# Kernel tuning notes

Hardware: AMD Instinct MI355X
Metric: run time of the kernel (lower is better)

The kernel has to match this reference:

```python
import jax, jax.numpy as jnp
import numpy as np

K = 3  # polynomial filter order

def gfgcn_layer(X, S, W, h, b):
    # X: [N, in], W: [in, out], h: [K], b: [out]
    X = X @ W
    X_out = h[0] * X
    Sx = X
    for k in range(1, K):
        Sx = S @ Sx                 # graph shift propagation
        X_out = X_out + h[k] * Sx   # scalar-weighted accumulate
    return X_out + b[None, :]


def setup_inputs() -> dict:
    key = jax.random.key(0)
    ks = jax.random.split(key, 12)
    N, in_dim, hid_dim, out_dim = 8192, 512, 128, 64
    # scale S so repeated propagation stays numerically tame
    S = jax.random.normal(ks[0], (N, N), dtype=jnp.float32) / jnp.sqrt(jnp.float32(N))
    X = jax.random.normal(ks[1], (N, in_dim), dtype=jnp.float32)
    def kaiming(k, shape):
        bound = np.sqrt(6.0 / shape[0])
        return jax.random.uniform(k, shape, jnp.float32, -bound, bound)
    W1 = kaiming(ks[2], (in_dim, hid_dim))
    W2 = kaiming(ks[3], (hid_dim, hid_dim))
    W3 = kaiming(ks[4], (hid_dim, out_dim))
    h1 = jnp.ones((K,), jnp.float32)
    h2 = jnp.ones((K,), jnp.float32)
    h3 = jnp.ones((K,), jnp.float32)
    b1 = jnp.zeros((hid_dim,), jnp.float32)
    b2 = jnp.zeros((hid_dim,), jnp.float32)
    b3 = jnp.zeros((out_dim,), jnp.float32)
    return {"S": S, "X": X, "W1": W1, "h1": h1, "b1": b1,
            "W2": W2, "h2": h2, "b2": b2, "W3": W3, "h3": h3, "b3": b3}


def reference(S, X, W1, h1, b1, W2, h2, b2, W3, h3, b3):
    # layer 1 + ReLU (dropout p=0 -> identity, batch_norm=False)
    X = jax.nn.relu(gfgcn_layer(X, S, W1, h1, b1))
    # layer 2 + ReLU
    X = jax.nn.relu(gfgcn_layer(X, S, W2, h2, b2))
    # last layer, last_act = Identity
    return gfgcn_layer(X, S, W3, h3, b3)
```

## Files before the change

### kernel.cpp

```cpp
#include <hip/hip_runtime.h>


typedef __attribute__((ext_vector_type(4))) float  f32x4;
typedef __attribute__((ext_vector_type(8))) __bf16 bf16x8;
typedef __attribute__((ext_vector_type(4))) __bf16 bf16x4;

__device__ __forceinline__ void gload_lds16(const __bf16* g, __bf16* l) {
    __builtin_amdgcn_global_load_lds(
        (const __attribute__((address_space(1))) void*)g,
        (__attribute__((address_space(3))) void*)l, 16, 0, 0);
}

__global__ void cvt_f32_bf16(const float4* __restrict__ in,
                             bf16x4* __restrict__ out, int n4) {
    int i  = blockIdx.x * blockDim.x + threadIdx.x;
    int st = gridDim.x * blockDim.x;
    for (; i < n4; i += st) {
        float4 v = in[i];
        bf16x4 o;
        o[0] = (__bf16)v.x; o[1] = (__bf16)v.y;
        o[2] = (__bf16)v.z; o[3] = (__bf16)v.w;
        out[i] = o;
    }
}

__global__ void cvt_transpose(const float* __restrict__ W,
                              __bf16* __restrict__ Wt, int Kd, int Md) {
    int i = blockIdx.x * blockDim.x + threadIdx.x;
    if (i < Kd * Md) {
        int k = i / Md, m = i % Md;
        Wt[(size_t)m * Kd + k] = (__bf16)W[i];
    }
}

template<int MF, int NF, int OUTMODE>
__global__ __launch_bounds__(256)
void gemm_rd(const __bf16* __restrict__ A, const __bf16* __restrict__ Bt,
             void* __restrict__ out, int K, int Kchunk, int Mtot, int Ntot)
{
    const int lane = threadIdx.x & 63;
    const int w    = threadIdx.x >> 6;
    const int l15  = lane & 15;
    const int quad = lane >> 4;

    const int m_base = blockIdx.x * (64 * MF) + w * (16 * MF);
    const int n_base = blockIdx.y * (16 * NF);
    const int kstart = blockIdx.z * Kchunk;

    const __bf16* Ap[MF];
    #pragma unroll
    for (int mf = 0; mf < MF; mf++)
        Ap[mf] = A + (size_t)(m_base + mf * 16 + l15) * K + kstart + quad * 8;
    const __bf16* Bp[NF];
    #pragma unroll
    for (int nf = 0; nf < NF; nf++)
        Bp[nf] = Bt + (size_t)(n_base + nf * 16 + l15) * K + kstart + quad * 8;

    f32x4 acc[MF][NF];
    #pragma unroll
    for (int mf = 0; mf < MF; mf++)
        #pragma unroll
        for (int nf = 0; nf < NF; nf++)
            acc[mf][nf] = (f32x4){0.f, 0.f, 0.f, 0.f};

    #pragma unroll 2
    for (int ks = 0; ks < Kchunk; ks += 32) {
        bf16x8 a[MF], b[NF];
        #pragma unroll
        for (int mf = 0; mf < MF; mf++) a[mf] = *(const bf16x8*)(Ap[mf] + ks);
        #pragma unroll
        for (int nf = 0; nf < NF; nf++) b[nf] = *(const bf16x8*)(Bp[nf] + ks);
        #pragma unroll
        for (int mf = 0; mf < MF; mf++)
            #pragma unroll
            for (int nf = 0; nf < NF; nf++)
                acc[mf][nf] = __builtin_amdgcn_mfma_f32_16x16x32_bf16(
                    a[mf], b[nf], acc[mf][nf], 0, 0, 0);
    }

    if (OUTMODE == 0) {
        float* P = (float*)out + (size_t)blockIdx.z * Mtot * Ntot;
        #pragma unroll
        for (int mf = 0; mf < MF; mf++) {
            const int rowb = m_base + mf * 16 + quad * 4;
            #pragma unroll
            for (int nf = 0; nf < NF; nf++) {
                const int col = n_base + nf * 16 + l15;
                *(f32x4*)(P + (size_t)col * Mtot + rowb) = acc[mf][nf];
            }
        }
    } else {
        __bf16* O = (__bf16*)out;
        #pragma unroll
        for (int mf = 0; mf < MF; mf++) {
            const int rowb = m_base + mf * 16 + quad * 4;
            #pragma unroll
            for (int nf = 0; nf < NF; nf++) {
                const int col = n_base + nf * 16 + l15;
                #pragma unroll
                for (int r = 0; r < 4; r++)
                    O[(size_t)(rowb + r) * Ntot + col] = (__bf16)acc[mf][nf][r];
            }
        }
    }
}

template<int NF>
__global__ __launch_bounds__(256)
void sgemm_lds(const __bf16* __restrict__ A, const __bf16* __restrict__ Bt,
               float* __restrict__ P, int K, int Kchunk, int Mtot, int Ntot)
{
    __shared__ __bf16 Asm[2][128 * 32];
    __shared__ __bf16 Bsm[2][NF * 16 * 32];

    const int t    = threadIdx.x;
    const int lane = t & 63;
    const int w    = t >> 6;
    const int l15  = lane & 15;
    const int quad = lane >> 4;

    const int m_block = blockIdx.x * 128;
    const int kstart  = blockIdx.z * Kchunk;

    const __bf16* gA = A  + (size_t)(m_block + (t >> 2)) * K + kstart + (t & 3) * 8;
    const __bf16* gB = Bt + (size_t)(t >> 2) * K + kstart + (t & 3) * 8;

    f32x4 acc[2][NF];
    #pragma unroll
    for (int mf = 0; mf < 2; mf++)
        #pragma unroll
        for (int nf = 0; nf < NF; nf++)
            acc[mf][nf] = (f32x4){0.f, 0.f, 0.f, 0.f};

    auto stage = [&](int buf, int ks) {
        gload_lds16(gA + ks,                   &Asm[buf][t * 8]);
        gload_lds16(gA + (size_t)64 * K + ks,  &Asm[buf][2048 + t * 8]);
        gload_lds16(gB + ks,                   &Bsm[buf][t * 8]);
        if (NF == 8)
            gload_lds16(gB + (size_t)64 * K + ks, &Bsm[buf][2048 + t * 8]);
    };

    stage(0, 0);
    __syncthreads();

    int buf = 0;
    for (int ks = 0; ; ) {
        const int nks = ks + 32;
        if (nks < Kchunk) stage(buf ^ 1, nks);

        bf16x8 a0, a1, b[NF];
        const int arow = w * 32 + l15;
        a0 = *(const bf16x8*)&Asm[buf][(arow)      * 32 + quad * 8];
        a1 = *(const bf16x8*)&Asm[buf][(arow + 16) * 32 + quad * 8];
        #pragma unroll
        for (int nf = 0; nf < NF; nf++)
            b[nf] = *(const bf16x8*)&Bsm[buf][(nf * 16 + l15) * 32 + quad * 8];

        #pragma unroll
        for (int nf = 0; nf < NF; nf++)
            acc[0][nf] = __builtin_amdgcn_mfma_f32_16x16x32_bf16(a0, b[nf], acc[0][nf], 0, 0, 0);
        #pragma unroll
        for (int nf = 0; nf < NF; nf++)
            acc[1][nf] = __builtin_amdgcn_mfma_f32_16x16x32_bf16(a1, b[nf], acc[1][nf], 0, 0, 0);

        ks = nks;
        if (ks >= Kchunk) break;
        __syncthreads();
        buf ^= 1;
    }

    float* Pz = P + (size_t)blockIdx.z * Mtot * Ntot;
    #pragma unroll
    for (int mf = 0; mf < 2; mf++) {
        const int rowb = m_block + w * 32 + mf * 16 + quad * 4;
        #pragma unroll
        for (int nf = 0; nf < NF; nf++) {
            const int col = nf * 16 + l15;
            *(f32x4*)(Pz + (size_t)col * Mtot + rowb) = acc[mf][nf];
        }
    }
    (void)Ntot;
}

__global__ void reduce_partials(const float* __restrict__ P,
                                __bf16* __restrict__ Y, int total4,
                                int SP, int MN) {
    int i = blockIdx.x * blockDim.x + threadIdx.x;
    if (i >= total4) return;
    size_t base = (size_t)i * 4;
    float4 s = *(const float4*)(P + base);
    for (int sp = 1; sp < SP; sp++) {
        float4 v = *(const float4*)(P + (size_t)sp * MN + base);
        s.x += v.x; s.y += v.y; s.z += v.z; s.w += v.w;
    }
    bf16x4 o; o[0] = (__bf16)s.x; o[1] = (__bf16)s.y;
    o[2] = (__bf16)s.z; o[3] = (__bf16)s.w;
    *(bf16x4*)(Y + base) = o;
}

template<int RELU, int F32OUT>
__global__ void combine_out(const float* __restrict__ P,
                            const __bf16* __restrict__ Y0t,
                            const __bf16* __restrict__ Y1t,
                            const float* __restrict__ h,
                            const float* __restrict__ bias,
                            void* __restrict__ outp,
                            int F, int SP) {
    const int i = blockIdx.x * blockDim.x + threadIdx.x;
    const int total = F * 2048;
    if (i >= total) return;
    const int f  = i >> 11;
    const int n4 = i & 2047;
    const size_t base = (size_t)f * 8192 + (size_t)n4 * 4;
    const int MN = F * 8192;

    float4 s = *(const float4*)(P + base);
    for (int sp = 1; sp < SP; sp++) {
        float4 v = *(const float4*)(P + (size_t)sp * MN + base);
        s.x += v.x; s.y += v.y; s.z += v.z; s.w += v.w;
    }
    bf16x4 y0 = *(const bf16x4*)(Y0t + base);
    bf16x4 y1 = *(const bf16x4*)(Y1t + base);
    const float h0 = h[0], h1 = h[1], h2 = h[2], bb = bias[f];

    float v[4] = {s.x, s.y, s.z, s.w};
    #pragma unroll
    for (int r = 0; r < 4; r++) {
        float x = h0 * (float)y0[r] + h1 * (float)y1[r] + h2 * v[r] + bb;
        if (RELU) x = fmaxf(x, 0.0f);
        v[r] = x;
    }
    const int node = n4 * 4;
    if (F32OUT) {
        float* O = (float*)outp;
        #pragma unroll
        for (int r = 0; r < 4; r++) O[(size_t)(node + r) * F + f] = v[r];
    } else {
        __bf16* O = (__bf16*)outp;
        #pragma unroll
        for (int r = 0; r < 4; r++) O[(size_t)(node + r) * F + f] = (__bf16)v[r];
    }
}

extern "C" void kernel_launch(void* const* d_in, const int* in_sizes, int n_in,
                              void* d_out, int out_size, void* d_ws, size_t ws_size,
                              hipStream_t stream) {
    const float* S  = (const float*)d_in[0];
    const float* X  = (const float*)d_in[1];
    const float* W1 = (const float*)d_in[2];
    const float* h1 = (const float*)d_in[3];
    const float* b1 = (const float*)d_in[4];
    const float* W2 = (const float*)d_in[5];
    const float* h2 = (const float*)d_in[6];
    const float* b2 = (const float*)d_in[7];
    const float* W3 = (const float*)d_in[8];
    const float* h3 = (const float*)d_in[9];
    const float* b3 = (const float*)d_in[10];
    float* out = (float*)d_out;

    const int Nn = 8192, IN = 512, HID = 128, OUT = 64;

    char* ws = (char*)d_ws;
    size_t off = 0;
    auto carve = [&](size_t bytes) -> void* {
        void* p = ws + off;
        off += (bytes + 255) & ~(size_t)255;
        return p;
    };
    __bf16* Sb  = (__bf16*)carve((size_t)Nn * Nn  * 2);
    __bf16* Xb  = (__bf16*)carve((size_t)Nn * IN  * 2);
    __bf16* W1t = (__bf16*)carve((size_t)IN  * HID * 2);
    __bf16* W2t = (__bf16*)carve((size_t)HID * HID * 2);
    __bf16* W3t = (__bf16*)carve((size_t)HID * OUT * 2);
    __bf16* Y0t = (__bf16*)carve((size_t)HID * Nn * 2);
    __bf16* Y1t = (__bf16*)carve((size_t)HID * Nn * 2);
    __bf16* Act = (__bf16*)carve((size_t)Nn * HID * 2);
    size_t  base = off;

    const size_t per_split = (size_t)HID * Nn * 4;
    int SP = 1;
    while (SP < 8 && base + (size_t)(SP * 2) * per_split <= ws_size) SP *= 2;
    float* P = (float*)carve((size_t)SP * per_split);
    const int KCH = Nn / SP;

    {
        int n4 = Nn * Nn / 4;
        cvt_f32_bf16<<<dim3((n4 + 255) / 256), dim3(256), 0, stream>>>(
            (const float4*)S, (bf16x4*)Sb, n4);
        n4 = Nn * IN / 4;
        cvt_f32_bf16<<<dim3((n4 + 255) / 256), dim3(256), 0, stream>>>(
            (const float4*)X, (bf16x4*)Xb, n4);
    }
    cvt_transpose<<<dim3((IN * HID + 255) / 256), dim3(256), 0, stream>>>(W1, W1t, IN, HID);
    cvt_transpose<<<dim3((HID * HID + 255) / 256), dim3(256), 0, stream>>>(W2, W2t, HID, HID);
    cvt_transpose<<<dim3((HID * OUT + 255) / 256), dim3(256), 0, stream>>>(W3, W3t, HID, OUT);

    auto sgemm = [&](const __bf16* Bt, int F) {
        if (F == 128)
            sgemm_lds<8><<<dim3(Nn / 128, 1, SP), dim3(256), 0, stream>>>(
                Sb, Bt, P, Nn, KCH, Nn, F);
        else
            sgemm_lds<4><<<dim3(Nn / 128, 1, SP), dim3(256), 0, stream>>>(
                Sb, Bt, P, Nn, KCH, Nn, F);
    };
    auto reduceY = [&](__bf16* Y, int F) {
        int t4 = F * 2048;
        reduce_partials<<<dim3((t4 + 255) / 256), dim3(256), 0, stream>>>(
            P, Y, t4, SP, F * Nn);
    };

    gemm_rd<2, 4, 1><<<dim3(1, Nn / 64, 1), dim3(256), 0, stream>>>(
        W1t, Xb, Y0t, IN, IN, HID, Nn);
    sgemm(Y0t, HID);
    reduceY(Y1t, HID);
    sgemm(Y1t, HID);
    combine_out<1, 0><<<dim3(HID * 2048 / 256), dim3(256), 0, stream>>>(
        P, Y0t, Y1t, h1, b1, Act, HID, SP);

    gemm_rd<2, 4, 1><<<dim3(1, Nn / 64, 1), dim3(256), 0, stream>>>(
        W2t, Act, Y0t, HID, HID, HID, Nn);
    sgemm(Y0t, HID);
    reduceY(Y1t, HID);
    sgemm(Y1t, HID);
    combine_out<1, 0><<<dim3(HID * 2048 / 256), dim3(256), 0, stream>>>(
        P, Y0t, Y1t, h2, b2, Act, HID, SP);

    gemm_rd<1, 4, 1><<<dim3(1, Nn / 64, 1), dim3(256), 0, stream>>>(
        W3t, Act, Y0t, HID, HID, OUT, Nn);
    sgemm(Y0t, OUT);
    reduceY(Y1t, OUT);
    sgemm(Y1t, OUT);
    combine_out<0, 1><<<dim3(OUT * 2048 / 256), dim3(256), 0, stream>>>(
        P, Y0t, Y1t, h3, b3, out, OUT, SP);

    (void)in_sizes; (void)n_in; (void)out_size;
}
```

Baseline: 702.2 us.

## Retile S-propagation GEMM to 64-row blocks with 2x2 warps and swizzled LDS

Changes the S@X GEMM tile from 128 rows per block with warps splitting only M to 64 rows per block with a 2x2 warp grid over M and N. Each block now stages a 64xK A tile plus the full B tile. An XOR swizzle is applied to the LDS layout, both when loading into LDS and when reading from it, to cut bank conflicts. The grid doubles in size for more parallelism, at the cost of re-reading B from global memory twice as often per output row.

```diff
diff --git a/kernel.cpp b/kernel.cpp
--- a/kernel.cpp
+++ b/kernel.cpp
@@ -105,40 +105,57 @@
     }
 }
 
-template<int NF>
+template<int NFW>
 __global__ __launch_bounds__(256)
 void sgemm_lds(const __bf16* __restrict__ A, const __bf16* __restrict__ Bt,
-               float* __restrict__ P, int K, int Kchunk, int Mtot, int Ntot)
+               float* __restrict__ P, int K, int Kchunk, int Mtot)
 {
-    __shared__ __bf16 Asm[2][128 * 32];
-    __shared__ __bf16 Bsm[2][NF * 16 * 32];
+    constexpr int BN = 32 * NFW;
+    __shared__ __bf16 Asm[2][64 * 32];
+    __shared__ __bf16 Bsm[2][BN * 32];
 
     const int t    = threadIdx.x;
     const int lane = t & 63;
     const int w    = t >> 6;
+    const int wm   = w >> 1;
+    const int wn   = w & 1;
     const int l15  = lane & 15;
     const int quad = lane >> 4;
 
-    const int m_block = blockIdx.x * 128;
+    const int m_block = blockIdx.x * 64;
     const int kstart  = blockIdx.z * Kchunk;
 
-    const __bf16* gA = A  + (size_t)(m_block + (t >> 2)) * K + kstart + (t & 3) * 8;
-    const __bf16* gB = Bt + (size_t)(t >> 2) * K + kstart + (t & 3) * 8;
-
-    f32x4 acc[2][NF];
+    const int rt  = t >> 2;
+    const int qs  = (t & 3) ^ ((rt >> 1) & 3);
+    const __bf16* gA  = A  + (size_t)(m_block + rt) * K + kstart + qs * 8;
+    const __bf16* gB0 = Bt + (size_t)rt * K        + kstart + qs * 8;
+    const __bf16* gB1 = Bt + (size_t)(64 + rt) * K + kstart + qs * 8;
+
+    f32x4 acc[2][NFW];
     #pragma unroll
     for (int mf = 0; mf < 2; mf++)
         #pragma unroll
-        for (int nf = 0; nf < NF; nf++)
+        for (int nf = 0; nf < NFW; nf++)
             acc[mf][nf] = (f32x4){0.f, 0.f, 0.f, 0.f};
 
     auto stage = [&](int buf, int ks) {
-        gload_lds16(gA + ks,                   &Asm[buf][t * 8]);
-        gload_lds16(gA + (size_t)64 * K + ks,  &Asm[buf][2048 + t * 8]);
-        gload_lds16(gB + ks,                   &Bsm[buf][t * 8]);
-        if (NF == 8)
-            gload_lds16(gB + (size_t)64 * K + ks, &Bsm[buf][2048 + t * 8]);
+        gload_lds16(gA  + ks, &Asm[buf][t * 8]);
+        gload_lds16(gB0 + ks, &Bsm[buf][t * 8]);
+        if (NFW == 4)
+            gload_lds16(gB1 + ks, &Bsm[buf][2048 + t * 8]);
     };
+
+    int aoff[2], boff[NFW];
+    #pragma unroll
+    for (int mf = 0; mf < 2; mf++) {
+        const int ar = wm * 32 + mf * 16 + l15;
+        aoff[mf] = ar * 32 + (quad ^ ((ar >> 1) & 3)) * 8;
+    }
+    #pragma unroll
+    for (int nf = 0; nf < NFW; nf++) {
+        const int br = wn * 16 * NFW + nf * 16 + l15;
+        boff[nf] = br * 32 + (quad ^ ((br >> 1) & 3)) * 8;
+    }
 
     stage(0, 0);
     __syncthreads();
@@ -148,20 +165,20 @@
         const int nks = ks + 32;
         if (nks < Kchunk) stage(buf ^ 1, nks);
 
-        bf16x8 a0, a1, b[NF];
-        const int arow = w * 32 + l15;
-        a0 = *(const bf16x8*)&Asm[buf][(arow)      * 32 + quad * 8];
-        a1 = *(const bf16x8*)&Asm[buf][(arow + 16) * 32 + quad * 8];
-        #pragma unroll
-        for (int nf = 0; nf < NF; nf++)
-            b[nf] = *(const bf16x8*)&Bsm[buf][(nf * 16 + l15) * 32 + quad * 8];
-
-        #pragma unroll
-        for (int nf = 0; nf < NF; nf++)
-            acc[0][nf] = __builtin_amdgcn_mfma_f32_16x16x32_bf16(a0, b[nf], acc[0][nf], 0, 0, 0);
-        #pragma unroll
-        for (int nf = 0; nf < NF; nf++)
-            acc[1][nf] = __builtin_amdgcn_mfma_f32_16x16x32_bf16(a1, b[nf], acc[1][nf], 0, 0, 0);
+        bf16x8 a[2], b[NFW];
+        #pragma unroll
+        for (int mf = 0; mf < 2; mf++)
+            a[mf] = *(const bf16x8*)&Asm[buf][aoff[mf]];
+        #pragma unroll
+        for (int nf = 0; nf < NFW; nf++)
+            b[nf] = *(const bf16x8*)&Bsm[buf][boff[nf]];
+
+        #pragma unroll
+        for (int mf = 0; mf < 2; mf++)
+            #pragma unroll
+            for (int nf = 0; nf < NFW; nf++)
+                acc[mf][nf] = __builtin_amdgcn_mfma_f32_16x16x32_bf16(
+                    a[mf], b[nf], acc[mf][nf], 0, 0, 0);
 
         ks = nks;
         if (ks >= Kchunk) break;
@@ -169,17 +186,16 @@
         buf ^= 1;
     }
 
-    float* Pz = P + (size_t)blockIdx.z * Mtot * Ntot;
+    float* Pz = P + (size_t)blockIdx.z * Mtot * BN;
     #pragma unroll
     for (int mf = 0; mf < 2; mf++) {
-        const int rowb = m_block + w * 32 + mf * 16 + quad * 4;
-        #pragma unroll
-        for (int nf = 0; nf < NF; nf++) {
-            const int col = nf * 16 + l15;
+        const int rowb = m_block + wm * 32 + mf * 16 + quad * 4;
+        #pragma unroll
+        for (int nf = 0; nf < NFW; nf++) {
+            const int col = wn * 16 * NFW + nf * 16 + l15;
             *(f32x4*)(Pz + (size_t)col * Mtot + rowb) = acc[mf][nf];
         }
     }
-    (void)Ntot;
 }
 
 __global__ void reduce_partials(const float* __restrict__ P,
@@ -297,11 +313,11 @@
 
     auto sgemm = [&](const __bf16* Bt, int F) {
         if (F == 128)
-            sgemm_lds<8><<<dim3(Nn / 128, 1, SP), dim3(256), 0, stream>>>(
-                Sb, Bt, P, Nn, KCH, Nn, F);
+            sgemm_lds<4><<<dim3(Nn / 64, 1, SP), dim3(256), 0, stream>>>(
+                Sb, Bt, P, Nn, KCH, Nn);
         else
-            sgemm_lds<4><<<dim3(Nn / 128, 1, SP), dim3(256), 0, stream>>>(
-                Sb, Bt, P, Nn, KCH, Nn, F);
+            sgemm_lds<2><<<dim3(Nn / 64, 1, SP), dim3(256), 0, stream>>>(
+                Sb, Bt, P, Nn, KCH, Nn);
     };
     auto reduceY = [&](__bf16* Y, int F) {
         int t4 = F * 2048;
```

Result: no change. 710.4 us (+1.2%).
